# Optimization experiments

Measured on AMD Instinct MI355X. Metric: run time of the kernel, lower is better.

Reference implementation:

```python
import jax, jax.numpy as jnp
import numpy as np

R, C, N, E = 1, 4, 10000, 160000
H, EF, L, OUT = 128, 16, 3, 64


def _gelu(v):
    # torch F.gelu default = exact erf gelu
    return jax.nn.gelu(v, approximate=False)


def setup_inputs() -> dict:
    key = jax.random.key(0)
    ks = jax.random.split(key, 16)
    s = 0.05
    return {
        "x": jax.random.normal(ks[0], (R, C, N, H), jnp.float32),
        "node_mask": jax.random.uniform(ks[1], (R, C, N, 1), jnp.float32),
        "edge_attr": jax.random.normal(ks[2], (E, EF), jnp.float32),
        "bondW": jax.random.normal(ks[3], (EF, H), jnp.float32) * s,
        "bondb": jnp.zeros((H,), jnp.float32),
        "convW1": jax.random.normal(ks[4], (L, H, H), jnp.float32) * s,
        "convb1": jnp.zeros((L, H), jnp.float32),
        "convW2": jax.random.normal(ks[5], (L, H, H), jnp.float32) * s,
        "convb2": jnp.zeros((L, H), jnp.float32),
        "eps": jnp.zeros((L,), jnp.float32),
        "mlpW1": jax.random.normal(ks[6], (H, H), jnp.float32) * s,
        "mlpb1": jnp.zeros((H,), jnp.float32),
        "mlpW2": jax.random.normal(ks[7], (H, OUT), jnp.float32) * s,
        "mlpb2": jnp.zeros((OUT,), jnp.float32),
        "edge_index": jax.random.randint(ks[8], (2, E), 0, N, jnp.int32),
        "batch": jnp.zeros((N,), jnp.int32),
    }


def reference(x, node_mask, edge_attr, bondW, bondb, convW1, convb1, convW2, convb2,
              eps, mlpW1, mlpb1, mlpW2, mlpb2, edge_index, batch):
    src, dst = edge_index[0], edge_index[1]
    # shared bond encoder (Linear), broadcast to [1,1,E,H]
    edge_emb = edge_attr @ bondW + bondb                      # [E, H]
    # edge_weight = node_mask gathered at both endpoints      # [R, C, E, 1]
    edge_mask = node_mask[:, :, src, :] * node_mask[:, :, dst, :]
    for l in range(L):
        # gather-add-GELU-weight-scatter message passing
        msg = _gelu(x[:, :, src, :] + edge_emb) * edge_mask   # [R, C, E, H]
        agg = jnp.zeros_like(x).at[:, :, dst, :].add(msg)     # scatter_sum over dst
        h = (1.0 + eps[l]) * x + agg
        # conv mlp: Linear -> GELU -> Linear
        h = _gelu(h @ convW1[l] + convb1[l]) @ convW2[l] + convb2[l]
        h = _gelu(h)  # outer activation (norm=Identity, dropout=0)
        x = x + h     # residual
    # final MLP (num_mlp_layers=2, PyG MLP default relu act)
    y = jax.nn.relu(x @ mlpW1 + mlpb1) @ mlpW2 + mlpb2        # [R, C, N, OUT]
    denom = jax.lax.stop_gradient(node_mask).sum(axis=2)      # [R, C, 1]
    out = (y * node_mask).sum(axis=2) / denom                 # [R, C, OUT]
    return out
```

## Files before the change

### kernel.cpp

```cpp
#include <hip/hip_runtime.h>
#include <hip/hip_bf16.h>
#include <cstddef>
#include <cstdint>

#define NNODES 10000
#define NEDGES 160000
#define NH     128
#define NCOMBO 4
#define NMROWS (NCOMBO * NNODES)
#define FTILE  32
#define SSTR   136
#define FTILES (NMROWS / FTILE)

typedef __attribute__((ext_vector_type(8))) short short8v;
typedef __attribute__((ext_vector_type(4))) float f32x4;

__device__ __forceinline__ float gelu_f(float v) {
    const float u  = v * 0.70710678118654752f;
    float au = __builtin_fabsf(u);
    au = fminf(au, 3.9192f);
    const float t  = __builtin_amdgcn_rcpf(__builtin_fmaf(0.3275911f, au, 1.0f));
    const float e  = __builtin_amdgcn_exp2f(au * au * -1.4426950408889634f);
    float p = __builtin_fmaf(1.061405429f, t, -1.453152027f);
    p = __builtin_fmaf(p, t, 1.421413741f);
    p = __builtin_fmaf(p, t, -0.284496736f);
    p = __builtin_fmaf(p, t, 0.254829592f);
    const float erf_abs = 1.0f - p * t * e;
    const float erf_s   = __builtin_copysignf(erf_abs, v);
    return 0.5f * v * (1.0f + erf_s);
}

__device__ __forceinline__ uint16_t f2bf_rne(float f) {
    const uint32_t x = __float_as_uint(f);
    return (uint16_t)((x + 0x7fffu + ((x >> 16) & 1u)) >> 16);
}
__device__ __forceinline__ uint32_t packbf2(float lo, float hi) {
    return ((uint32_t)f2bf_rne(hi) << 16) | (uint32_t)f2bf_rne(lo);
}
__device__ __forceinline__ float bflo(uint32_t u) { return __uint_as_float(u << 16); }
__device__ __forceinline__ float bfhi(uint32_t u) { return __uint_as_float(u & 0xffff0000u); }

__global__ __launch_bounds__(256) void hist_kernel(const int* __restrict__ ei,
                                                   int* __restrict__ deg) {
    const int e = blockIdx.x * 256 + threadIdx.x;
    if (e < NEDGES) atomicAdd(&deg[ei[NEDGES + e]], 1);
}

__global__ __launch_bounds__(1024) void scan_kernel(const int* __restrict__ deg,
                                                    int* __restrict__ off,
                                                    int* __restrict__ cursor) {
    __shared__ int ssum[1024];
    const int tid  = threadIdx.x;
    const int base = tid * 10;
    int loc[10];
    int s = 0;
    #pragma unroll
    for (int i = 0; i < 10; ++i) {
        const int idx = base + i;
        loc[i] = s;
        s += (idx < NNODES) ? deg[idx] : 0;
    }
    ssum[tid] = s;
    for (int d = 1; d < 1024; d <<= 1) {
        __syncthreads();
        const int t = (tid >= d) ? ssum[tid - d] : 0;
        __syncthreads();
        ssum[tid] += t;
    }
    __syncthreads();
    const int pref = ssum[tid] - s;
    #pragma unroll
    for (int i = 0; i < 10; ++i) {
        const int idx = base + i;
        if (idx < NNODES) { off[idx] = pref + loc[i]; cursor[idx] = pref + loc[i]; }
    }
    if (tid == 0) off[NNODES] = NEDGES;
}

__global__ __launch_bounds__(256) void scatter_kernel(const int* __restrict__ ei,
                                                      const float* __restrict__ ea,
                                                      int* __restrict__ cursor,
                                                      int* __restrict__ esrc,
                                                      float* __restrict__ ea_s) {
    const int e = blockIdx.x * 256 + threadIdx.x;
    if (e < NEDGES) {
        const int src = ei[e];
        const int dst = ei[NEDGES + e];
        const int pos = atomicAdd(&cursor[dst], 1);
        esrc[pos] = src;
        const float4* s = reinterpret_cast<const float4*>(ea + (size_t)e * 16);
        float4*       d = reinterpret_cast<float4*>(ea_s + (size_t)pos * 16);
        d[0] = s[0]; d[1] = s[1]; d[2] = s[2]; d[3] = s[3];
    }
}

__global__ __launch_bounds__(256) void emb_kernel(
    const float* __restrict__ ea_s, const float* __restrict__ bW,
    const float* __restrict__ bb, uint32_t* __restrict__ embq)
{
    const int lane = threadIdx.x & 63;
    const int wid  = threadIdx.x >> 6;
    const int c0   = lane * 2;
    float2 wc[16];
    #pragma unroll
    for (int k = 0; k < 16; ++k)
        wc[k] = *reinterpret_cast<const float2*>(&bW[k * 128 + c0]);
    const float2 bbr = *reinterpret_cast<const float2*>(&bb[c0]);

    for (int j = blockIdx.x * 4 + wid; j < NEDGES; j += gridDim.x * 4) {
        const float4* eap = reinterpret_cast<const float4*>(ea_s + (size_t)j * 16);
        const float4 a0 = eap[0], a1 = eap[1], a2 = eap[2], a3 = eap[3];
        float s0 = bbr.x, s1 = bbr.y;
        s0 += a0.x*wc[0].x + a0.y*wc[1].x + a0.z*wc[2].x + a0.w*wc[3].x
            + a1.x*wc[4].x + a1.y*wc[5].x + a1.z*wc[6].x + a1.w*wc[7].x
            + a2.x*wc[8].x + a2.y*wc[9].x + a2.z*wc[10].x + a2.w*wc[11].x
            + a3.x*wc[12].x + a3.y*wc[13].x + a3.z*wc[14].x + a3.w*wc[15].x;
        s1 += a0.x*wc[0].y + a0.y*wc[1].y + a0.z*wc[2].y + a0.w*wc[3].y
            + a1.x*wc[4].y + a1.y*wc[5].y + a1.z*wc[6].y + a1.w*wc[7].y
            + a2.x*wc[8].y + a2.y*wc[9].y + a2.z*wc[10].y + a2.w*wc[11].y
            + a3.x*wc[12].y + a3.y*wc[13].y + a3.z*wc[14].y + a3.w*wc[15].y;
        embq[(size_t)j * 64 + lane] = packbf2(s0, s1);
    }
}

__global__ __launch_bounds__(256) void wtrans_kernel(
    const float* __restrict__ cW1, const float* __restrict__ cW2,
    const float* __restrict__ mW1, const float* __restrict__ mW2,
    short* __restrict__ wbf)
{
    const int gidx = blockIdx.x * 256 + threadIdx.x;
    if (gidx >= 122880) return;
    if (gidx < 114688) {
        const int m  = gidx >> 14;
        const int el = gidx & 16383;
        const int n  = el >> 7;
        const int k  = el & 127;
        const float* W = (m < 3) ? (cW1 + m * 16384)
                       : (m < 6) ? (cW2 + (m - 3) * 16384) : mW1;
        wbf[(size_t)m * 16384 + n * 128 + k] = (short)f2bf_rne(W[k * 128 + n]);
    } else {
        const int el = gidx - 114688;
        const int n  = el >> 7;
        const int k  = el & 127;
        wbf[114688 + n * 128 + k] = (short)f2bf_rne(mW2[k * 64 + n]);
    }
}

__global__ __launch_bounds__(256) void emsk_kernel(
    const float* __restrict__ nm, const int* __restrict__ off,
    const int* __restrict__ esrc, float4* __restrict__ emsk)
{
    const int n = blockIdx.x * 256 + threadIdx.x;
    if (n >= NNODES) return;
    const float d0 = nm[0 * NNODES + n], d1 = nm[1 * NNODES + n];
    const float d2 = nm[2 * NNODES + n], d3 = nm[3 * NNODES + n];
    const int j1 = off[n + 1];
    for (int j = off[n]; j < j1; ++j) {
        const int s = esrc[j];
        emsk[j] = make_float4(nm[0 * NNODES + s] * d0, nm[1 * NNODES + s] * d1,
                              nm[2 * NNODES + s] * d2, nm[3 * NNODES + s] * d3);
    }
}

__global__ __launch_bounds__(256) void xcast_kernel(const float* __restrict__ x,
                                                    uint32_t* __restrict__ xbf) {
    const int i = blockIdx.x * 256 + threadIdx.x;
    if (i < NMROWS * 64) {
        const float2 v = *reinterpret_cast<const float2*>(&x[(size_t)i * 2]);
        xbf[i] = packbf2(v.x, v.y);
    }
}

__global__ __launch_bounds__(256) void agg2_kernel(
    const uint32_t* __restrict__ xbf,
    const uint32_t* __restrict__ embq,
    const float4* __restrict__ emsk,
    const int*   __restrict__ off,
    const int*   __restrict__ esrc,
    const float* __restrict__ epsp, int layer,
    uint32_t* __restrict__ hbf)
{
    const int lane = threadIdx.x & 63;
    const int wid  = threadIdx.x >> 6;
    const float epv = 1.0f + epsp[layer];

    for (int n = blockIdx.x * 4 + wid; n < NNODES; n += gridDim.x * 4) {
        const int j0 = off[n], j1 = off[n + 1];
        float acc[4][2] = {{0.f,0.f},{0.f,0.f},{0.f,0.f},{0.f,0.f}};

        uint32_t eq_c = 0; uint32_t xu_c[4]; float4 em_c = {0,0,0,0};
        if (j0 < j1) {
            const int s = esrc[j0];
            eq_c = embq[(size_t)j0 * 64 + lane];
            em_c = emsk[j0];
            #pragma unroll
            for (int c = 0; c < 4; ++c)
                xu_c[c] = xbf[((size_t)c * NNODES + s) * 64 + lane];
        }
        for (int j = j0; j < j1; ++j) {
            const uint32_t eq = eq_c;
            const float4 em = em_c;
            uint32_t xu[4];
            #pragma unroll
            for (int c = 0; c < 4; ++c) xu[c] = xu_c[c];
            if (j + 1 < j1) {
                const int s = esrc[j + 1];
                eq_c = embq[(size_t)(j + 1) * 64 + lane];
                em_c = emsk[j + 1];
                #pragma unroll
                for (int c = 0; c < 4; ++c)
                    xu_c[c] = xbf[((size_t)c * NNODES + s) * 64 + lane];
            }
            const float e0 = bflo(eq);
            const float e1 = bfhi(eq);
            const float ms[4] = {em.x, em.y, em.z, em.w};
            #pragma unroll
            for (int c = 0; c < 4; ++c) {
                acc[c][0] += gelu_f(bflo(xu[c]) + e0) * ms[c];
                acc[c][1] += gelu_f(bfhi(xu[c]) + e1) * ms[c];
            }
        }
        #pragma unroll
        for (int c = 0; c < 4; ++c) {
            const uint32_t u = xbf[((size_t)c * NNODES + n) * 64 + lane];
            const float o0 = epv * bflo(u) + acc[c][0];
            const float o1 = epv * bfhi(u) + acc[c][1];
            hbf[((size_t)c * NNODES + n) * 64 + lane] = packbf2(o0, o1);
        }
    }
}

__global__ __launch_bounds__(256) void agg_kernel(
    const float* __restrict__ xcur, const float* __restrict__ nm,
    const float* __restrict__ ea_s, const float* __restrict__ bW,
    const float* __restrict__ bb, const int* __restrict__ off,
    const int* __restrict__ esrc, const float* __restrict__ epsp, int layer,
    short* __restrict__ hbf_s)
{
    const int tid = threadIdx.x;
    const int h   = tid & 127;
    const int sub = tid >> 7;
    float wc[16];
    #pragma unroll
    for (int k = 0; k < 16; ++k) wc[k] = bW[k * 128 + h];
    const float bbr = bb[h];
    const float epv = 1.0f + epsp[layer];

    for (int n = blockIdx.x * 2 + sub; n < NNODES; n += gridDim.x * 2) {
        float acc0 = 0.f, acc1 = 0.f, acc2 = 0.f, acc3 = 0.f;
        const int j0 = off[n], j1 = off[n + 1];
        const float d0 = nm[0*NNODES+n], d1 = nm[1*NNODES+n];
        const float d2 = nm[2*NNODES+n], d3 = nm[3*NNODES+n];
        for (int j = j0; j < j1; ++j) {
            const int src = esrc[j];
            const float4* eap = reinterpret_cast<const float4*>(ea_s + (size_t)j * 16);
            const float4 a0 = eap[0], a1 = eap[1], a2 = eap[2], a3 = eap[3];
            float emb = bbr;
            emb += a0.x*wc[0] + a0.y*wc[1] + a0.z*wc[2] + a0.w*wc[3];
            emb += a1.x*wc[4] + a1.y*wc[5] + a1.z*wc[6] + a1.w*wc[7];
            emb += a2.x*wc[8] + a2.y*wc[9] + a2.z*wc[10] + a2.w*wc[11];
            emb += a3.x*wc[12] + a3.y*wc[13] + a3.z*wc[14] + a3.w*wc[15];
            const float m0 = nm[0*NNODES+src]*d0, m1 = nm[1*NNODES+src]*d1;
            const float m2 = nm[2*NNODES+src]*d2, m3 = nm[3*NNODES+src]*d3;
            acc0 += gelu_f(xcur[((size_t)0*NNODES+src)*NH+h] + emb) * m0;
            acc1 += gelu_f(xcur[((size_t)1*NNODES+src)*NH+h] + emb) * m1;
            acc2 += gelu_f(xcur[((size_t)2*NNODES+src)*NH+h] + emb) * m2;
            acc3 += gelu_f(xcur[((size_t)3*NNODES+src)*NH+h] + emb) * m3;
        }
        hbf_s[((size_t)0*NNODES+n)*NH+h] = (short)f2bf_rne(epv * xcur[((size_t)0*NNODES+n)*NH+h] + acc0);
        hbf_s[((size_t)1*NNODES+n)*NH+h] = (short)f2bf_rne(epv * xcur[((size_t)1*NNODES+n)*NH+h] + acc1);
        hbf_s[((size_t)2*NNODES+n)*NH+h] = (short)f2bf_rne(epv * xcur[((size_t)2*NNODES+n)*NH+h] + acc2);
        hbf_s[((size_t)3*NNODES+n)*NH+h] = (short)f2bf_rne(epv * xcur[((size_t)3*NNODES+n)*NH+h] + acc3);
    }
}

__global__ __launch_bounds__(256) void conv_mfma_kernel(
    const uint32_t* __restrict__ hb,
    const float* __restrict__ resid,
    const short* __restrict__ W1t, const float* __restrict__ b1,
    const short* __restrict__ W2t, const float* __restrict__ b2,
    float* __restrict__ outp,
    short* __restrict__ xb_s)
{
    __shared__ short sh[FTILE * SSTR];
    __shared__ short st[FTILE * SSTR];
    __shared__ short sw[128 * SSTR];

    const int tid  = threadIdx.x;
    const int lane = tid & 63;
    const int w    = tid >> 6;
    const int l15  = lane & 15;
    const int l4   = lane >> 4;
    const int colb = w * 32;
    const int row0 = blockIdx.x * FTILE;

    for (int i = tid; i < FTILE * 16; i += 256) {
        const int r = i >> 4, c = i & 15;
        *reinterpret_cast<uint4*>(&sh[r * SSTR + c * 8]) =
            *reinterpret_cast<const uint4*>(&hb[(size_t)(row0 + r) * 64 + c * 4]);
    }
    for (int i = tid; i < 128 * 16; i += 256) {
        const int r = i >> 4, c = i & 15;
        *reinterpret_cast<uint4*>(&sw[r * SSTR + c * 8]) =
            *reinterpret_cast<const uint4*>(&W1t[r * 128 + c * 8]);
    }
    __syncthreads();

    f32x4 a00 = {0,0,0,0}, a01 = {0,0,0,0}, a10 = {0,0,0,0}, a11 = {0,0,0,0};
    #pragma unroll
    for (int s = 0; s < 4; ++s) {
        const int ko = s * 32 + l4 * 8;
        short8v fa0 = *reinterpret_cast<const short8v*>(&sh[(l15)      * SSTR + ko]);
        short8v fa1 = *reinterpret_cast<const short8v*>(&sh[(16 + l15) * SSTR + ko]);
        short8v fb0 = *reinterpret_cast<const short8v*>(&sw[(colb + l15)      * SSTR + ko]);
        short8v fb1 = *reinterpret_cast<const short8v*>(&sw[(colb + 16 + l15) * SSTR + ko]);
        a00 = __builtin_amdgcn_mfma_f32_16x16x32_bf16(fa0, fb0, a00, 0, 0, 0);
        a01 = __builtin_amdgcn_mfma_f32_16x16x32_bf16(fa0, fb1, a01, 0, 0, 0);
        a10 = __builtin_amdgcn_mfma_f32_16x16x32_bf16(fa1, fb0, a10, 0, 0, 0);
        a11 = __builtin_amdgcn_mfma_f32_16x16x32_bf16(fa1, fb1, a11, 0, 0, 0);
    }

    {
        const float bv0 = b1[colb + l15];
        const float bv1 = b1[colb + 16 + l15];
        #pragma unroll
        for (int j = 0; j < 4; ++j) {
            const int r0 = l4 * 4 + j;
            st[r0 * SSTR + colb + l15]             = (short)f2bf_rne(gelu_f(a00[j] + bv0));
            st[r0 * SSTR + colb + 16 + l15]        = (short)f2bf_rne(gelu_f(a01[j] + bv1));
            st[(16 + r0) * SSTR + colb + l15]      = (short)f2bf_rne(gelu_f(a10[j] + bv0));
            st[(16 + r0) * SSTR + colb + 16 + l15] = (short)f2bf_rne(gelu_f(a11[j] + bv1));
        }
    }
    __syncthreads();

    for (int i = tid; i < 128 * 16; i += 256) {
        const int r = i >> 4, c = i & 15;
        *reinterpret_cast<uint4*>(&sw[r * SSTR + c * 8]) =
            *reinterpret_cast<const uint4*>(&W2t[r * 128 + c * 8]);
    }
    __syncthreads();

    a00 = {0,0,0,0}; a01 = {0,0,0,0}; a10 = {0,0,0,0}; a11 = {0,0,0,0};
    #pragma unroll
    for (int s = 0; s < 4; ++s) {
        const int ko = s * 32 + l4 * 8;
        short8v fa0 = *reinterpret_cast<const short8v*>(&st[(l15)      * SSTR + ko]);
        short8v fa1 = *reinterpret_cast<const short8v*>(&st[(16 + l15) * SSTR + ko]);
        short8v fb0 = *reinterpret_cast<const short8v*>(&sw[(colb + l15)      * SSTR + ko]);
        short8v fb1 = *reinterpret_cast<const short8v*>(&sw[(colb + 16 + l15) * SSTR + ko]);
        a00 = __builtin_amdgcn_mfma_f32_16x16x32_bf16(fa0, fb0, a00, 0, 0, 0);
        a01 = __builtin_amdgcn_mfma_f32_16x16x32_bf16(fa0, fb1, a01, 0, 0, 0);
        a10 = __builtin_amdgcn_mfma_f32_16x16x32_bf16(fa1, fb0, a10, 0, 0, 0);
        a11 = __builtin_amdgcn_mfma_f32_16x16x32_bf16(fa1, fb1, a11, 0, 0, 0);
    }

    {
        const float bv0 = b2[colb + l15];
        const float bv1 = b2[colb + 16 + l15];
        #pragma unroll
        for (int j = 0; j < 4; ++j) {
            const int r0 = row0 + l4 * 4 + j;
            const int r1 = r0 + 16;
            const size_t o00 = (size_t)r0 * NH + colb + l15;
            const size_t o01 = (size_t)r0 * NH + colb + 16 + l15;
            const size_t o10 = (size_t)r1 * NH + colb + l15;
            const size_t o11 = (size_t)r1 * NH + colb + 16 + l15;
            const float v00 = resid[o00] + gelu_f(a00[j] + bv0);
            const float v01 = resid[o01] + gelu_f(a01[j] + bv1);
            const float v10 = resid[o10] + gelu_f(a10[j] + bv0);
            const float v11 = resid[o11] + gelu_f(a11[j] + bv1);
            outp[o00] = v00; xb_s[o00] = (short)f2bf_rne(v00);
            outp[o01] = v01; xb_s[o01] = (short)f2bf_rne(v01);
            outp[o10] = v10; xb_s[o10] = (short)f2bf_rne(v10);
            outp[o11] = v11; xb_s[o11] = (short)f2bf_rne(v11);
        }
    }
}

__global__ __launch_bounds__(256) void mlp_mfma_kernel(
    const uint32_t* __restrict__ xb,
    const short* __restrict__ W1t, const float* __restrict__ b1,
    const short* __restrict__ W2t,
    const float* __restrict__ b2,
    const float* __restrict__ nm,
    float* __restrict__ oacc)
{
    __shared__ short sx[FTILE * SSTR];
    __shared__ short st[FTILE * SSTR];
    __shared__ short sw[128 * SSTR];
    __shared__ float sacc[256];

    const int tid  = threadIdx.x;
    const int lane = tid & 63;
    const int w    = tid >> 6;
    const int l15  = lane & 15;
    const int l4   = lane >> 4;
    const int colb = w * 32;
    const int row0 = blockIdx.x * FTILE;

    sacc[tid] = 0.0f;

    for (int i = tid; i < FTILE * 16; i += 256) {
        const int r = i >> 4, c = i & 15;
        *reinterpret_cast<uint4*>(&sx[r * SSTR + c * 8]) =
            *reinterpret_cast<const uint4*>(&xb[(size_t)(row0 + r) * 64 + c * 4]);
    }
    for (int i = tid; i < 128 * 16; i += 256) {
        const int r = i >> 4, c = i & 15;
        *reinterpret_cast<uint4*>(&sw[r * SSTR + c * 8]) =
            *reinterpret_cast<const uint4*>(&W1t[r * 128 + c * 8]);
    }
    __syncthreads();

    f32x4 a00 = {0,0,0,0}, a01 = {0,0,0,0}, a10 = {0,0,0,0}, a11 = {0,0,0,0};
    #pragma unroll
    for (int s = 0; s < 4; ++s) {
        const int ko = s * 32 + l4 * 8;
        short8v fa0 = *reinterpret_cast<const short8v*>(&sx[(l15)      * SSTR + ko]);
        short8v fa1 = *reinterpret_cast<const short8v*>(&sx[(16 + l15) * SSTR + ko]);
        short8v fb0 = *reinterpret_cast<const short8v*>(&sw[(colb + l15)      * SSTR + ko]);
        short8v fb1 = *reinterpret_cast<const short8v*>(&sw[(colb + 16 + l15) * SSTR + ko]);
        a00 = __builtin_amdgcn_mfma_f32_16x16x32_bf16(fa0, fb0, a00, 0, 0, 0);
        a01 = __builtin_amdgcn_mfma_f32_16x16x32_bf16(fa0, fb1, a01, 0, 0, 0);
        a10 = __builtin_amdgcn_mfma_f32_16x16x32_bf16(fa1, fb0, a10, 0, 0, 0);
        a11 = __builtin_amdgcn_mfma_f32_16x16x32_bf16(fa1, fb1, a11, 0, 0, 0);
    }

    {
        const float bv0 = b1[colb + l15];
        const float bv1 = b1[colb + 16 + l15];
        #pragma unroll
        for (int j = 0; j < 4; ++j) {
            const int r0 = l4 * 4 + j;
            st[r0 * SSTR + colb + l15]             = (short)f2bf_rne(fmaxf(a00[j] + bv0, 0.f));
            st[r0 * SSTR + colb + 16 + l15]        = (short)f2bf_rne(fmaxf(a01[j] + bv1, 0.f));
            st[(16 + r0) * SSTR + colb + l15]      = (short)f2bf_rne(fmaxf(a10[j] + bv0, 0.f));
            st[(16 + r0) * SSTR + colb + 16 + l15] = (short)f2bf_rne(fmaxf(a11[j] + bv1, 0.f));
        }
    }
    __syncthreads();

    for (int i = tid; i < 64 * 16; i += 256) {
        const int r = i >> 4, c = i & 15;
        *reinterpret_cast<uint4*>(&sw[r * SSTR + c * 8]) =
            *reinterpret_cast<const uint4*>(&W2t[r * 128 + c * 8]);
    }
    __syncthreads();

    const int colb2 = w * 16;
    f32x4 c0f = {0,0,0,0}, c1f = {0,0,0,0};
    #pragma unroll
    for (int s = 0; s < 4; ++s) {
        const int ko = s * 32 + l4 * 8;
        short8v fa0 = *reinterpret_cast<const short8v*>(&st[(l15)      * SSTR + ko]);
        short8v fa1 = *reinterpret_cast<const short8v*>(&st[(16 + l15) * SSTR + ko]);
        short8v fb  = *reinterpret_cast<const short8v*>(&sw[(colb2 + l15) * SSTR + ko]);
        c0f = __builtin_amdgcn_mfma_f32_16x16x32_bf16(fa0, fb, c0f, 0, 0, 0);
        c1f = __builtin_amdgcn_mfma_f32_16x16x32_bf16(fa1, fb, c1f, 0, 0, 0);
    }

    {
        const float bv = b2[colb2 + l15];
        #pragma unroll
        for (int j = 0; j < 4; ++j) {
            const int gr0 = row0 + l4 * 4 + j;
            const int gr1 = gr0 + 16;
            const float w0 = nm[gr0];
            const float w1 = nm[gr1];
            const int cb0 = gr0 / NNODES;
            const int cb1 = gr1 / NNODES;
            atomicAdd(&sacc[cb0 * 64 + colb2 + l15], (c0f[j] + bv) * w0);
            atomicAdd(&sacc[cb1 * 64 + colb2 + l15], (c1f[j] + bv) * w1);
        }
    }

    __syncthreads();
    atomicAdd(&oacc[tid], sacc[tid]);
}

__global__ __launch_bounds__(256) void final_kernel(
    const float* __restrict__ acc, const float* __restrict__ nm,
    float* __restrict__ outp)
{
    const int tid  = threadIdx.x;
    const int c    = tid >> 6;
    const int lane = tid & 63;
    float s = 0.f;
    for (int n = lane; n < NNODES; n += 64) s += nm[c * NNODES + n];
    #pragma unroll
    for (int off = 32; off > 0; off >>= 1) s += __shfl_down(s, off, 64);
    const float denom = __shfl(s, 0, 64);
    outp[tid] = acc[tid] / denom;
}

extern "C" void kernel_launch(void* const* d_in, const int* in_sizes, int n_in,
                              void* d_out, int out_size, void* d_ws, size_t ws_size,
                              hipStream_t stream) {
    const float* x    = (const float*)d_in[0];
    const float* nm   = (const float*)d_in[1];
    const float* ea   = (const float*)d_in[2];
    const float* bW   = (const float*)d_in[3];
    const float* bb   = (const float*)d_in[4];
    const float* cW1  = (const float*)d_in[5];
    const float* cb1  = (const float*)d_in[6];
    const float* cW2  = (const float*)d_in[7];
    const float* cb2  = (const float*)d_in[8];
    const float* eps  = (const float*)d_in[9];
    const float* mW1  = (const float*)d_in[10];
    const float* mb1  = (const float*)d_in[11];
    const float* mW2  = (const float*)d_in[12];
    const float* mb2  = (const float*)d_in[13];
    const int*   ei   = (const int*)d_in[14];

    float* ws = (float*)d_ws;
    const bool big = ws_size >= (size_t)23230600ULL * 4ULL;

    if (big) {
        float*    xcur = ws;
        float*    oacc = ws + 5120000;
        uint32_t* hbf  = (uint32_t*)(ws + 5120512);
        uint32_t* xbf  = (uint32_t*)(ws + 7680512);
        float*    ea_s = ws + 10240512;
        short*    wbf  = (short*)ea_s;
        float4*   emsk = (float4*)(ea_s + 61440);
        uint32_t* embq = (uint32_t*)(ws + 12800512);
        int*      ib   = (int*)(ws + 23040512);
        int* off = ib; int* cur = ib + 10002; int* deg = ib + 20002;
        int* esrc = ib + 30002;

        hipMemsetAsync(deg, 0, 10000 * 4, stream);
        hist_kernel<<<(NEDGES + 255) / 256, 256, 0, stream>>>(ei, deg);
        scan_kernel<<<1, 1024, 0, stream>>>(deg, off, cur);
        scatter_kernel<<<(NEDGES + 255) / 256, 256, 0, stream>>>(ei, ea, cur, esrc, ea_s);
        emb_kernel<<<10000, 256, 0, stream>>>(ea_s, bW, bb, embq);
        wtrans_kernel<<<480, 256, 0, stream>>>(cW1, cW2, mW1, mW2, wbf);
        emsk_kernel<<<(NNODES + 255) / 256, 256, 0, stream>>>(nm, off, esrc, emsk);
        xcast_kernel<<<10000, 256, 0, stream>>>(x, xbf);

        for (int l = 0; l < 3; ++l) {
            const float* resid = (l == 0) ? x : xcur;
            agg2_kernel<<<2500, 256, 0, stream>>>(xbf, embq, emsk, off, esrc,
                                                  eps, l, hbf);
            conv_mfma_kernel<<<FTILES, 256, 0, stream>>>(hbf, resid,
                wbf + (size_t)l * 16384, cb1 + l * 128,
                wbf + (size_t)(3 + l) * 16384, cb2 + l * 128,
                xcur, (short*)xbf);
        }
        hipMemsetAsync(oacc, 0, 256 * 4, stream);
        mlp_mfma_kernel<<<FTILES, 256, 0, stream>>>(xbf, wbf + 98304, mb1,
                                                    wbf + 114688, mb2, nm, oacc);
        final_kernel<<<1, 256, 0, stream>>>(oacc, nm, (float*)d_out);
    } else {
        float*    xcur = ws;
        float*    oacc = ws + 5120000;
        uint32_t* hbf  = (uint32_t*)(ws + 5120512);
        uint32_t* xbf  = (uint32_t*)(ws + 7680512);
        float*    ea_s = ws + 10240512;
        int*      ib   = (int*)(ws + 12800512);
        int* off = ib; int* cur = ib + 10002; int* deg = ib + 20002;
        int* esrc = ib + 30002;
        short* wbf = (short*)(ib + 190004);

        hipMemcpyAsync(xcur, x, (size_t)5120000 * 4, hipMemcpyDeviceToDevice, stream);
        hipMemsetAsync(deg, 0, 10000 * 4, stream);
        hist_kernel<<<(NEDGES + 255) / 256, 256, 0, stream>>>(ei, deg);
        scan_kernel<<<1, 1024, 0, stream>>>(deg, off, cur);
        scatter_kernel<<<(NEDGES + 255) / 256, 256, 0, stream>>>(ei, ea, cur, esrc, ea_s);
        wtrans_kernel<<<480, 256, 0, stream>>>(cW1, cW2, mW1, mW2, wbf);

        for (int l = 0; l < 3; ++l) {
            const float* resid = (l == 0) ? x : xcur;
            agg_kernel<<<2500, 256, 0, stream>>>(xcur, nm, ea_s, bW, bb, off, esrc,
                                                 eps, l, (short*)hbf);
            conv_mfma_kernel<<<FTILES, 256, 0, stream>>>(hbf, resid,
                wbf + (size_t)l * 16384, cb1 + l * 128,
                wbf + (size_t)(3 + l) * 16384, cb2 + l * 128,
                xcur, (short*)xbf);
        }
        hipMemsetAsync(oacc, 0, 256 * 4, stream);
        mlp_mfma_kernel<<<FTILES, 256, 0, stream>>>(xbf, wbf + 98304, mb1,
                                                    wbf + 114688, mb2, nm, oacc);
        final_kernel<<<1, 256, 0, stream>>>(oacc, nm, (float*)d_out);
    }
}
```

Measured before the change: 437.4 us.

## Fuse prep kernels into one launch and prefetch edge source indices two ahead

Merges the x-cast, weight-transpose and edge-mask kernels into a single block-range-dispatched prep kernel, removing two launches and their gaps. In the aggregation kernel, edge source indices are now loaded two edges ahead, so the dependent index load is off the critical path of the gather prefetch. The small path now also runs the x cast into xbf, which it did not need before and which adds some memory traffic.

```diff
diff --git a/kernel.cpp b/kernel.cpp
--- a/kernel.cpp
+++ b/kernel.cpp
@@ -123,51 +123,49 @@
     }
 }
 
-__global__ __launch_bounds__(256) void wtrans_kernel(
+__global__ __launch_bounds__(256) void prep_kernel(
+    const float* __restrict__ x, uint32_t* __restrict__ xbf,
     const float* __restrict__ cW1, const float* __restrict__ cW2,
     const float* __restrict__ mW1, const float* __restrict__ mW2,
-    short* __restrict__ wbf)
-{
-    const int gidx = blockIdx.x * 256 + threadIdx.x;
-    if (gidx >= 122880) return;
-    if (gidx < 114688) {
-        const int m  = gidx >> 14;
-        const int el = gidx & 16383;
-        const int n  = el >> 7;
-        const int k  = el & 127;
-        const float* W = (m < 3) ? (cW1 + m * 16384)
-                       : (m < 6) ? (cW2 + (m - 3) * 16384) : mW1;
-        wbf[(size_t)m * 16384 + n * 128 + k] = (short)f2bf_rne(W[k * 128 + n]);
-    } else {
-        const int el = gidx - 114688;
-        const int n  = el >> 7;
-        const int k  = el & 127;
-        wbf[114688 + n * 128 + k] = (short)f2bf_rne(mW2[k * 64 + n]);
-    }
-}
-
-__global__ __launch_bounds__(256) void emsk_kernel(
+    short* __restrict__ wbf,
     const float* __restrict__ nm, const int* __restrict__ off,
     const int* __restrict__ esrc, float4* __restrict__ emsk)
 {
-    const int n = blockIdx.x * 256 + threadIdx.x;
-    if (n >= NNODES) return;
-    const float d0 = nm[0 * NNODES + n], d1 = nm[1 * NNODES + n];
-    const float d2 = nm[2 * NNODES + n], d3 = nm[3 * NNODES + n];
-    const int j1 = off[n + 1];
-    for (int j = off[n]; j < j1; ++j) {
-        const int s = esrc[j];
-        emsk[j] = make_float4(nm[0 * NNODES + s] * d0, nm[1 * NNODES + s] * d1,
-                              nm[2 * NNODES + s] * d2, nm[3 * NNODES + s] * d3);
-    }
-}
-
-__global__ __launch_bounds__(256) void xcast_kernel(const float* __restrict__ x,
-                                                    uint32_t* __restrict__ xbf) {
-    const int i = blockIdx.x * 256 + threadIdx.x;
-    if (i < NMROWS * 64) {
-        const float2 v = *reinterpret_cast<const float2*>(&x[(size_t)i * 2]);
-        xbf[i] = packbf2(v.x, v.y);
+    const int b = blockIdx.x;
+    if (b < 10000) {
+        const int i = b * 256 + threadIdx.x;
+        if (i < NMROWS * 64) {
+            const float2 v = *reinterpret_cast<const float2*>(&x[(size_t)i * 2]);
+            xbf[i] = packbf2(v.x, v.y);
+        }
+    } else if (b < 10480) {
+        const int gidx = (b - 10000) * 256 + threadIdx.x;
+        if (gidx >= 122880) return;
+        if (gidx < 114688) {
+            const int m  = gidx >> 14;
+            const int el = gidx & 16383;
+            const int n  = el >> 7;
+            const int k  = el & 127;
+            const float* W = (m < 3) ? (cW1 + m * 16384)
+                           : (m < 6) ? (cW2 + (m - 3) * 16384) : mW1;
+            wbf[(size_t)m * 16384 + n * 128 + k] = (short)f2bf_rne(W[k * 128 + n]);
+        } else {
+            const int el = gidx - 114688;
+            const int n  = el >> 7;
+            const int k  = el & 127;
+            wbf[114688 + n * 128 + k] = (short)f2bf_rne(mW2[k * 64 + n]);
+        }
+    } else {
+        const int n = (b - 10480) * 256 + threadIdx.x;
+        if (n >= NNODES) return;
+        const float d0 = nm[0 * NNODES + n], d1 = nm[1 * NNODES + n];
+        const float d2 = nm[2 * NNODES + n], d3 = nm[3 * NNODES + n];
+        const int j1 = off[n + 1];
+        for (int j = off[n]; j < j1; ++j) {
+            const int s = esrc[j];
+            emsk[j] = make_float4(nm[0 * NNODES + s] * d0, nm[1 * NNODES + s] * d1,
+                                  nm[2 * NNODES + s] * d2, nm[3 * NNODES + s] * d3);
+        }
     }
 }
 
@@ -188,14 +186,16 @@
         const int j0 = off[n], j1 = off[n + 1];
         float acc[4][2] = {{0.f,0.f},{0.f,0.f},{0.f,0.f},{0.f,0.f}};
 
+        int sA = (j0     < j1) ? esrc[j0]     : 0;
+        int sB = (j0 + 1 < j1) ? esrc[j0 + 1] : 0;
+
         uint32_t eq_c = 0; uint32_t xu_c[4]; float4 em_c = {0,0,0,0};
         if (j0 < j1) {
-            const int s = esrc[j0];
             eq_c = embq[(size_t)j0 * 64 + lane];
             em_c = emsk[j0];
             #pragma unroll
             for (int c = 0; c < 4; ++c)
-                xu_c[c] = xbf[((size_t)c * NNODES + s) * 64 + lane];
+                xu_c[c] = xbf[((size_t)c * NNODES + sA) * 64 + lane];
         }
         for (int j = j0; j < j1; ++j) {
             const uint32_t eq = eq_c;
@@ -203,13 +203,15 @@
             uint32_t xu[4];
             #pragma unroll
             for (int c = 0; c < 4; ++c) xu[c] = xu_c[c];
+
+            sA = sB;
+            sB = (j + 2 < j1) ? esrc[j + 2] : 0;
             if (j + 1 < j1) {
-                const int s = esrc[j + 1];
                 eq_c = embq[(size_t)(j + 1) * 64 + lane];
                 em_c = emsk[j + 1];
                 #pragma unroll
                 for (int c = 0; c < 4; ++c)
-                    xu_c[c] = xbf[((size_t)c * NNODES + s) * 64 + lane];
+                    xu_c[c] = xbf[((size_t)c * NNODES + sA) * 64 + lane];
             }
             const float e0 = bflo(eq);
             const float e1 = bfhi(eq);
@@ -534,9 +536,8 @@
         scan_kernel<<<1, 1024, 0, stream>>>(deg, off, cur);
         scatter_kernel<<<(NEDGES + 255) / 256, 256, 0, stream>>>(ei, ea, cur, esrc, ea_s);
         emb_kernel<<<10000, 256, 0, stream>>>(ea_s, bW, bb, embq);
-        wtrans_kernel<<<480, 256, 0, stream>>>(cW1, cW2, mW1, mW2, wbf);
-        emsk_kernel<<<(NNODES + 255) / 256, 256, 0, stream>>>(nm, off, esrc, emsk);
-        xcast_kernel<<<10000, 256, 0, stream>>>(x, xbf);
+        prep_kernel<<<10520, 256, 0, stream>>>(x, xbf, cW1, cW2, mW1, mW2, wbf,
+                                               nm, off, esrc, emsk);
 
         for (int l = 0; l < 3; ++l) {
             const float* resid = (l == 0) ? x : xcur;
@@ -567,7 +568,8 @@
         hist_kernel<<<(NEDGES + 255) / 256, 256, 0, stream>>>(ei, deg);
         scan_kernel<<<1, 1024, 0, stream>>>(deg, off, cur);
         scatter_kernel<<<(NEDGES + 255) / 256, 256, 0, stream>>>(ei, ea, cur, esrc, ea_s);
-        wtrans_kernel<<<480, 256, 0, stream>>>(cW1, cW2, mW1, mW2, wbf);
+        prep_kernel<<<10480, 256, 0, stream>>>(x, xbf, cW1, cW2, mW1, mW2, wbf,
+                                               nm, off, esrc, nullptr);
 
         for (int l = 0; l < 3; ++l) {
             const float* resid = (l == 0) ? x : xcur;
```

After: 442.8 us. Within noise of the previous version (+1.2%).
